# Performance work log

Hardware: AMD Instinct MI355X
Metric: run time of the kernel (lower is better)

Reference implementation:

```python
import jax, jax.numpy as jnp
import numpy as np

LORA_RANK = 16
LORA_ALPHA = 16
LORA_SCALE = LORA_ALPHA / LORA_RANK


def setup_inputs() -> dict:
    key = jax.random.key(0)
    k1, k2, k3, k4, k5 = jax.random.split(key, 5)
    B, S, D_IN, D_OUT, N_LORA, R = 8, 2048, 4096, 4096, 3, LORA_RANK
    std = 1.0 / np.sqrt(D_IN)
    x = jax.random.normal(k1, (B, S, D_IN), dtype=jnp.float32)
    weight = jax.random.truncated_normal(k2, -3.0, 3.0, (D_OUT, D_IN), dtype=jnp.float32) * std
    bias = jax.random.normal(k3, (D_OUT,), dtype=jnp.float32) * 0.01
    lora_A = jax.random.normal(k4, (N_LORA, R, D_IN), dtype=jnp.float32) * std
    lora_B = jax.random.normal(k5, (N_LORA, D_OUT, R), dtype=jnp.float32) * 0.02
    # segment starts: samples 0-1 -> no LoRA (index 0 reserved), 2-3 -> adapter 1, 4-5 -> adapter 2, 6-7 -> adapter 3
    lora_start_indices = jnp.arange(4, dtype=jnp.int64) * 2
    return {"x": x, "weight": weight, "bias": bias, "lora_A": lora_A,
            "lora_B": lora_B, "lora_start_indices": lora_start_indices}


def reference(x, weight, bias, lora_A, lora_B, lora_start_indices):
    # Base linear: y = x @ W^T + b   (torch: weight @ x_column)
    y = jnp.einsum('bsd,od->bso', x, weight) + bias  # [B,S,D_out]
    B = x.shape[0]
    # Map each batch sample to its segment (SGMV-style dispatch over contiguous segments).
    seg = jnp.searchsorted(lora_start_indices, jnp.arange(B), side='right') - 1  # [B], 0 = no LoRA
    adapter_idx = jnp.clip(seg - 1, 0, lora_A.shape[0] - 1)
    A = lora_A[adapter_idx]   # [B, r, D_in]  (tiny gather)
    Bw = lora_B[adapter_idx]  # [B, D_out, r]
    lo = jnp.einsum('bsr,bor->bso', jnp.einsum('bsd,brd->bsr', x, A), Bw) * LORA_SCALE
    use_lora = (seg > 0)[:, None, None]
    return y + jnp.where(use_lora, lo, jnp.zeros((), dtype=y.dtype))
```

## Files before the change

kernel.cpp:

```cpp
#include <hip/hip_runtime.h>


typedef __attribute__((ext_vector_type(8))) short short8;
typedef __attribute__((ext_vector_type(4))) float f32x4;
typedef __attribute__((ext_vector_type(4))) unsigned short u16x4;
typedef unsigned short u16;

typedef __attribute__((address_space(1))) void as1_void;
typedef __attribute__((address_space(3))) void as3_void;

#define M_DIM 16384
#define N_DIM 4096
#define K_DIM 4096
#define K2 8192
#define BM 256
#define BN 256
#define BK 64

__device__ __forceinline__ u16 f2bf(float f) {
  union { float f; unsigned u; } v; v.f = f;
  unsigned r = (v.u + 0x7FFFu + ((v.u >> 16) & 1u)) >> 16;
  return (u16)r;
}
__device__ __forceinline__ float bf2f(u16 u) {
  union { unsigned u; float f; } v; v.u = ((unsigned)u) << 16;
  return v.f;
}
__device__ __forceinline__ void gload16(const void* g, void* lds) {
  __builtin_amdgcn_global_load_lds((as1_void*)g, (as3_void*)lds, 16, 0, 0);
}
__device__ __forceinline__ int seg_of_batch(const int* starts, int b) {
  int seg = -1;
#pragma unroll
  for (int i = 0; i < 4; ++i) seg += (starts[i] <= b) ? 1 : 0;
  return seg;
}

#define VMCNT(n) asm volatile("s_waitcnt vmcnt(" #n ")" ::: "memory")

__global__ __launch_bounds__(256) void prep_kernel(
    const float* __restrict__ x, const float* __restrict__ wgt,
    const float* __restrict__ lA, const float* __restrict__ lB,
    u16* __restrict__ xbf, u16* __restrict__ wbf,
    u16* __restrict__ abf, u16* __restrict__ bw) {
  const long long NX4 = 16777216LL;
  const long long NW4 = 4194304LL;
  const long long NA4 = 49152LL;
  const long long NB  = 12288LL;
  const long long total = NX4 + NW4 + NA4 + NB;
  const f32x4* x4 = (const f32x4*)x;
  const f32x4* w4 = (const f32x4*)wgt;
  const f32x4* a4 = (const f32x4*)lA;
  u16x4* xo = (u16x4*)xbf;
  u16x4* wo = (u16x4*)wbf;
  u16x4* ao = (u16x4*)abf;
  for (long long i = (long long)blockIdx.x * blockDim.x + threadIdx.x; i < total;
       i += (long long)gridDim.x * blockDim.x) {
    if (i < NX4) {
      f32x4 v = x4[i];
      u16x4 o = {f2bf(v.x), f2bf(v.y), f2bf(v.z), f2bf(v.w)};
      xo[i] = o;
    } else if (i < NX4 + NW4) {
      long long j = i - NX4;
      f32x4 v = w4[j];
      u16x4 o = {f2bf(v.x), f2bf(v.y), f2bf(v.z), f2bf(v.w)};
      wo[j] = o;
    } else if (i < NX4 + NW4 + NA4) {
      long long j = i - NX4 - NW4;
      f32x4 v = a4[j];
      u16x4 o = {f2bf(v.x), f2bf(v.y), f2bf(v.z), f2bf(v.w)};
      ao[j] = o;
    } else {
      long long p = i - NX4 - NW4 - NA4;
      const float* src = lB + p * 16;
      u16* dst = bw + p * 32;
#pragma unroll
      for (int j = 0; j < 16; ++j) dst[j] = f2bf(src[j]);
#pragma unroll
      for (int j = 16; j < 32; ++j) dst[j] = 0;
    }
  }
}

__global__ __launch_bounds__(256) void ucompute_kernel(
    const u16* __restrict__ xbf, const u16* __restrict__ abf,
    const int* __restrict__ starts, u16* __restrict__ u) {
  const int l = threadIdx.x & 63;
  const int w = threadIdx.x >> 6;
  const int mbase = blockIdx.x * 16 + w * 4;
  const int b = mbase >> 11;
  const int seg = seg_of_batch(starts, b);
  const int use = seg > 0;
  int ad = seg - 1; ad = ad < 0 ? 0 : (ad > 2 ? 2 : ad);

  float acc[4][16];
#pragma unroll
  for (int row = 0; row < 4; ++row)
#pragma unroll
    for (int r = 0; r < 16; ++r) acc[row][r] = 0.f;

  if (use) {
    const u16* xr = xbf + (size_t)mbase * K_DIM + l * 8;
    const u16* ar = abf + (size_t)ad * (16 * K_DIM) + l * 8;
    for (int pass = 0; pass < 8; ++pass) {
      const int off = pass * 512;
      float xv[4][8];
#pragma unroll
      for (int row = 0; row < 4; ++row) {
        short8 xs = *(const short8*)(xr + (size_t)row * K_DIM + off);
#pragma unroll
        for (int j = 0; j < 8; ++j) xv[row][j] = bf2f((u16)xs[j]);
      }
#pragma unroll
      for (int r = 0; r < 16; ++r) {
        short8 av = *(const short8*)(ar + (size_t)r * K_DIM + off);
#pragma unroll
        for (int j = 0; j < 8; ++j) {
          float a = bf2f((u16)av[j]);
#pragma unroll
          for (int row = 0; row < 4; ++row) acc[row][r] += xv[row][j] * a;
        }
      }
    }
  }
#pragma unroll
  for (int row = 0; row < 4; ++row) {
    float myval = 0.f;
#pragma unroll
    for (int r = 0; r < 16; ++r) {
      float v = acc[row][r];
      v += __shfl_xor(v, 32);
      v += __shfl_xor(v, 16);
      v += __shfl_xor(v, 8);
      v += __shfl_xor(v, 4);
      v += __shfl_xor(v, 2);
      v += __shfl_xor(v, 1);
      if (l == r) myval = v;
    }
    if (l < 32) u[(size_t)(mbase + row) * 32 + l] = (l < 16) ? f2bf(myval) : (u16)0;
  }
}


#define STAGE_A(buf, ih, kt) do { \
  gload16(aSrc + (size_t)((ih)*64) * K2 + (size_t)(kt)*128, \
          &As[buf][((ih)*64) * BK] + w * 512); \
  gload16(aSrc + (size_t)((ih)*64 + 128) * K2 + (size_t)(kt)*128, \
          &As[buf][((ih)*64 + 128) * BK] + w * 512); \
} while (0)
#define STAGE_B(buf, jh, kt) do { \
  gload16(bSrc + (size_t)((jh)*32) * K2 + (size_t)(kt)*128, \
          &Bs[buf][((jh)*32 + (w >> 2)*64) * BK] + (w & 3) * 512); \
  gload16(bSrc + (size_t)((jh)*32 + 128) * K2 + (size_t)(kt)*128, \
          &Bs[buf][((jh)*32 + (w >> 2)*64 + 128) * BK] + (w & 3) * 512); \
} while (0)

#define PHASE(buf, ih, jh, LA, LB, BARR, STAGE_STMT, WAIT_STMT) do { \
  if (LA) { \
    _Pragma("unroll") \
    for (int i2 = 0; i2 < 4; ++i2) { \
      const u16* ar = &As[buf][(wr*128 + (ih)*64 + i2*16 + fm) * BK]; \
      aFr[i2][0] = *(const short8*)(ar + c0); \
      aFr[i2][1] = *(const short8*)(ar + c1); \
    } \
  } \
  if (LB) { \
    _Pragma("unroll") \
    for (int j2 = 0; j2 < 2; ++j2) { \
      const u16* br = &Bs[buf][(wc*64 + (jh)*32 + j2*16 + fm) * BK]; \
      BARR[j2][0] = *(const short8*)(br + c0); \
      BARR[j2][1] = *(const short8*)(br + c1); \
    } \
  } \
  STAGE_STMT; \
  WAIT_STMT; \
  __builtin_amdgcn_s_barrier(); \
  __builtin_amdgcn_s_setprio(1); \
  _Pragma("unroll") \
  for (int i2 = 0; i2 < 4; ++i2) \
  _Pragma("unroll") \
  for (int j2 = 0; j2 < 2; ++j2) { \
    acc[(ih)*4 + i2][(jh)*2 + j2] = __builtin_amdgcn_mfma_f32_16x16x32_bf16( \
        aFr[i2][0], BARR[j2][0], acc[(ih)*4 + i2][(jh)*2 + j2], 0, 0, 0); \
    acc[(ih)*4 + i2][(jh)*2 + j2] = __builtin_amdgcn_mfma_f32_16x16x32_bf16( \
        aFr[i2][1], BARR[j2][1], acc[(ih)*4 + i2][(jh)*2 + j2], 0, 0, 0); \
  } \
  __builtin_amdgcn_s_setprio(0); \
  __builtin_amdgcn_s_barrier(); \
} while (0)

__global__ __launch_bounds__(512, 2) void gemm8_kernel(
    const u16* __restrict__ xbf, const u16* __restrict__ wbf,
    const float* __restrict__ bias, const u16* __restrict__ ubuf,
    const u16* __restrict__ bwpad, const int* __restrict__ starts,
    float* __restrict__ out) {
  __shared__ u16 As[2][BM * BK];
  __shared__ u16 Bs[2][BN * BK];

  const int tid = threadIdx.x;
  const int l = tid & 63;
  const int w = tid >> 6;

  const int bid = blockIdx.x;
  const int nb = (bid & 7) * 128 + (bid >> 3);
  const int m0 = (nb >> 4) << 8;
  const int n0 = (nb & 15) << 8;

  const int b = m0 >> 11;
  const int seg = seg_of_batch(starts, b);
  int ad = seg - 1; ad = ad < 0 ? 0 : (ad > 2 ? 2 : ad);

  const int lrow = l >> 3;
  const int swzslot = (l & 7) ^ lrow;
  const char* aSrc = (const char*)xbf +
      (size_t)(m0 + 8 * w + lrow) * K2 + swzslot * 16;
  const char* bSrc = (const char*)wbf +
      (size_t)(n0 + (w >> 2) * 64 + (w & 3) * 8 + lrow) * K2 + swzslot * 16;

  const int fm = l & 15;
  const int q = l >> 4;
  const int wr = w >> 2;
  const int wc = w & 3;
  const int c0 = ((q ^ (fm & 7)) * 8);
  const int c1 = (((q + 4) ^ (fm & 7)) * 8);

  f32x4 acc[8][4];
  const f32x4 z4 = {0.f, 0.f, 0.f, 0.f};
#pragma unroll
  for (int i = 0; i < 8; ++i)
#pragma unroll
    for (int j = 0; j < 4; ++j) acc[i][j] = z4;

  short8 aFr[4][2];
  short8 bF0r[2][2];
  short8 bF1r[2][2];

  STAGE_A(0, 0, 0); STAGE_B(0, 0, 0); STAGE_B(0, 1, 0); STAGE_A(0, 1, 0);
  STAGE_A(1, 0, 1); STAGE_B(1, 1, 1); STAGE_A(1, 1, 1);
  VMCNT(6);
  __builtin_amdgcn_s_barrier();

  for (int s = 0; s < 32; ++s) {
    const int t1 = 2 * s + 1;
    const int t2 = 2 * s + 2;
    const int t3 = 2 * s + 3;
    const bool more = (s < 31);
    PHASE(0, 0, 0, 1, 1, bF0r, STAGE_B(1, 0, t1), (void)0);
    PHASE(0, 0, 1, 0, 1, bF1r, if (more) STAGE_A(0, 0, t2), (void)0);
    PHASE(0, 1, 1, 1, 0, bF1r, if (more) STAGE_B(0, 1, t2), (void)0);
    PHASE(0, 1, 0, 0, 0, bF0r, if (more) STAGE_A(0, 1, t2),
          if (more) VMCNT(6); else VMCNT(0));
    PHASE(1, 0, 0, 1, 1, bF0r, if (more) STAGE_B(0, 0, t2), (void)0);
    PHASE(1, 0, 1, 0, 1, bF1r, if (more) STAGE_A(1, 0, t3), (void)0);
    PHASE(1, 1, 1, 1, 0, bF1r, if (more) STAGE_B(1, 1, t3), (void)0);
    PHASE(1, 1, 0, 0, 0, bF0r, if (more) STAGE_A(1, 1, t3),
          if (more) VMCNT(6); else VMCNT(0));
  }

  {
    u16* la = &As[0][0];
    u16* lb = &Bs[0][0];
    const int ls = l & 3;
    const int lr = l >> 2;
    const char* uSrc = (const char*)ubuf +
        (size_t)(m0 + 16 * w + lr) * 64 + ls * 16;
    const char* vSrc = (const char*)bwpad +
        ((size_t)ad * N_DIM + n0 + 16 * w + lr) * 64 + ls * 16;
    gload16(uSrc, la + (16 * w) * 32);
    gload16(uSrc + (size_t)128 * 64, la + (128 + 16 * w) * 32);
    gload16(vSrc, lb + (16 * w) * 32);
    gload16(vSrc + (size_t)128 * 64, lb + (128 + 16 * w) * 32);
    VMCNT(0);
    __builtin_amdgcn_s_barrier();
    short8 aF[8], bF[4];
#pragma unroll
    for (int i = 0; i < 8; ++i)
      aF[i] = *(const short8*)(la + (wr * 128 + i * 16 + fm) * 32 + q * 8);
#pragma unroll
    for (int j = 0; j < 4; ++j)
      bF[j] = *(const short8*)(lb + (wc * 64 + j * 16 + fm) * 32 + q * 8);
#pragma unroll
    for (int i = 0; i < 8; ++i)
#pragma unroll
      for (int j = 0; j < 4; ++j)
        acc[i][j] = __builtin_amdgcn_mfma_f32_16x16x32_bf16(aF[i], bF[j],
                                                            acc[i][j], 0, 0, 0);
  }

  float bv[4];
#pragma unroll
  for (int j = 0; j < 4; ++j) bv[j] = bias[n0 + wc * 64 + j * 16 + fm];
#pragma unroll
  for (int i = 0; i < 8; ++i) {
#pragma unroll
    for (int ii = 0; ii < 4; ++ii) {
      const int m = m0 + wr * 128 + i * 16 + q * 4 + ii;
      float* orow = out + (size_t)m * N_DIM + n0 + wc * 64 + fm;
#pragma unroll
      for (int j = 0; j < 4; ++j) orow[j * 16] = acc[i][j][ii] + bv[j];
    }
  }
}

__global__ __launch_bounds__(256) void u_f32_kernel(
    const float* __restrict__ x, const float* __restrict__ lA,
    const int* __restrict__ starts, float* __restrict__ u) {
  const int l = threadIdx.x & 63;
  const int w = threadIdx.x >> 6;
  const int m = blockIdx.x * 4 + w;
  const int b = m >> 11;
  const int seg = seg_of_batch(starts, b);
  const int use = seg > 0;
  int ad = seg - 1; ad = ad < 0 ? 0 : (ad > 2 ? 2 : ad);
  float acc[16];
#pragma unroll
  for (int r = 0; r < 16; ++r) acc[r] = 0.f;
  if (use) {
    const float* xr = x + (size_t)m * K_DIM + l * 4;
    const float* ar = lA + (size_t)ad * (16 * K_DIM) + l * 4;
    for (int pass = 0; pass < 16; ++pass) {
      const int off = pass * 256;
      f32x4 xv = *(const f32x4*)(xr + off);
#pragma unroll
      for (int r = 0; r < 16; ++r) {
        f32x4 av = *(const f32x4*)(ar + (size_t)r * K_DIM + off);
        acc[r] += xv.x * av.x + xv.y * av.y + xv.z * av.z + xv.w * av.w;
      }
    }
  }
  float myval = 0.f;
#pragma unroll
  for (int r = 0; r < 16; ++r) {
    float v = acc[r];
    v += __shfl_xor(v, 32);
    v += __shfl_xor(v, 16);
    v += __shfl_xor(v, 8);
    v += __shfl_xor(v, 4);
    v += __shfl_xor(v, 2);
    v += __shfl_xor(v, 1);
    if (l == r) myval = v;
  }
  if (l < 16) u[(size_t)m * 16 + l] = myval;
}

__global__ __launch_bounds__(256) void gemm_f32_fallback(
    const float* __restrict__ x, const float* __restrict__ wgt,
    const float* __restrict__ bias, const float* __restrict__ lB,
    const float* __restrict__ u, const int* __restrict__ starts,
    float* __restrict__ out) {
  __shared__ float xs[4096];
  const int m = blockIdx.y;
  const int n0 = blockIdx.x * 256;
  const int t = threadIdx.x;
  const f32x4* xr4 = (const f32x4*)(x + (size_t)m * K_DIM);
  f32x4* xs4 = (f32x4*)xs;
  for (int i = t; i < 1024; i += 256) xs4[i] = xr4[i];
  __syncthreads();
  const int b = m >> 11;
  const int seg = seg_of_batch(starts, b);
  const int use = seg > 0;
  int ad = seg - 1; ad = ad < 0 ? 0 : (ad > 2 ? 2 : ad);
  const int n = n0 + t;
  const f32x4* wr = (const f32x4*)(wgt + (size_t)n * K_DIM);
  float acc = 0.f;
  for (int kk = 0; kk < 1024; ++kk) {
    f32x4 wv = wr[kk];
    f32x4 xv = xs4[kk];
    acc += xv.x * wv.x + xv.y * wv.y + xv.z * wv.z + xv.w * wv.w;
  }
  acc += bias[n];
  if (use) {
    const float* Bn = lB + ((size_t)ad * N_DIM + n) * 16;
    const float* um = u + (size_t)m * 16;
    float lo = 0.f;
#pragma unroll
    for (int r = 0; r < 16; ++r) lo += um[r] * Bn[r];
    acc += lo;
  }
  out[(size_t)m * N_DIM + n] = acc;
}

extern "C" void kernel_launch(void* const* d_in, const int* in_sizes, int n_in,
                              void* d_out, int out_size, void* d_ws, size_t ws_size,
                              hipStream_t stream) {
  const float* x    = (const float*)d_in[0];
  const float* wgt  = (const float*)d_in[1];
  const float* bias = (const float*)d_in[2];
  const float* lA   = (const float*)d_in[3];
  const float* lB   = (const float*)d_in[4];
  const int* starts = (const int*)d_in[5];
  float* out = (float*)d_out;

  const size_t XBF_OFF = 0;
  const size_t WBF_OFF = 134217728;
  const size_t ABF_OFF = 167772160;
  const size_t BW_OFF  = 168165376;
  const size_t U_OFF   = 168951808;
  const size_t WS_NEEDED = 170000384;

  if (ws_size >= WS_NEEDED) {
    u16* xbf = (u16*)((char*)d_ws + XBF_OFF);
    u16* wbf = (u16*)((char*)d_ws + WBF_OFF);
    u16* abf = (u16*)((char*)d_ws + ABF_OFF);
    u16* bw  = (u16*)((char*)d_ws + BW_OFF);
    u16* u   = (u16*)((char*)d_ws + U_OFF);
    prep_kernel<<<8192, 256, 0, stream>>>(x, wgt, lA, lB, xbf, wbf, abf, bw);
    ucompute_kernel<<<1024, 256, 0, stream>>>(xbf, abf, starts, u);
    gemm8_kernel<<<1024, 512, 0, stream>>>(xbf, wbf, bias, u, bw, starts, out);
  } else {
    float* uf = (float*)d_ws;
    u_f32_kernel<<<4096, 256, 0, stream>>>(x, lA, starts, uf);
    gemm_f32_fallback<<<dim3(16, 16384), 256, 0, stream>>>(x, wgt, bias, lB, uf, starts, out);
  }
}
```

Baseline: 1.132 ms.

## Software-pipeline LDS fragment reads one phase ahead of MFMA

Restructures the 8-phase GEMM main loop so LDS reads of A/B fragments for the next phase are issued before the current phase's MFMAs, using double-buffered register fragments (aF0r/aF1r, bF0A/bF0B). The aim is to hide LDS read latency behind matrix-core work instead of serializing reads, barrier and MFMA. This costs extra VGPRs for the additional fragment buffers, which at launch bounds (512,2) may cause spills. It also relies on the barrier placement correctly protecting buffers that are overwritten while reads are in flight.

```diff
diff --git a/kernel.cpp b/kernel.cpp
--- a/kernel.cpp
+++ b/kernel.cpp
@@ -37,6 +37,7 @@
 }
 
 #define VMCNT(n) asm volatile("s_waitcnt vmcnt(" #n ")" ::: "memory")
+#define BAR() __builtin_amdgcn_s_barrier()
 
 __global__ __launch_bounds__(256) void prep_kernel(
     const float* __restrict__ x, const float* __restrict__ wgt,
@@ -155,38 +156,35 @@
           &Bs[buf][((jh)*32 + (w >> 2)*64 + 128) * BK] + (w & 3) * 512); \
 } while (0)
 
-#define PHASE(buf, ih, jh, LA, LB, BARR, STAGE_STMT, WAIT_STMT) do { \
-  if (LA) { \
-    _Pragma("unroll") \
-    for (int i2 = 0; i2 < 4; ++i2) { \
-      const u16* ar = &As[buf][(wr*128 + (ih)*64 + i2*16 + fm) * BK]; \
-      aFr[i2][0] = *(const short8*)(ar + c0); \
-      aFr[i2][1] = *(const short8*)(ar + c1); \
-    } \
+#define READ_A(dst, buf, ih) do { \
+  _Pragma("unroll") \
+  for (int i2 = 0; i2 < 4; ++i2) { \
+    const u16* ar = &As[buf][(wr*128 + (ih)*64 + i2*16 + fm) * BK]; \
+    dst[i2][0] = *(const short8*)(ar + c0); \
+    dst[i2][1] = *(const short8*)(ar + c1); \
   } \
-  if (LB) { \
-    _Pragma("unroll") \
-    for (int j2 = 0; j2 < 2; ++j2) { \
-      const u16* br = &Bs[buf][(wc*64 + (jh)*32 + j2*16 + fm) * BK]; \
-      BARR[j2][0] = *(const short8*)(br + c0); \
-      BARR[j2][1] = *(const short8*)(br + c1); \
-    } \
+} while (0)
+#define READ_B(dst, buf, jh) do { \
+  _Pragma("unroll") \
+  for (int j2 = 0; j2 < 2; ++j2) { \
+    const u16* br = &Bs[buf][(wc*64 + (jh)*32 + j2*16 + fm) * BK]; \
+    dst[j2][0] = *(const short8*)(br + c0); \
+    dst[j2][1] = *(const short8*)(br + c1); \
   } \
-  STAGE_STMT; \
-  WAIT_STMT; \
-  __builtin_amdgcn_s_barrier(); \
+} while (0)
+
+#define MFMA16(ih, jh, A, B) do { \
   __builtin_amdgcn_s_setprio(1); \
   _Pragma("unroll") \
   for (int i2 = 0; i2 < 4; ++i2) \
   _Pragma("unroll") \
   for (int j2 = 0; j2 < 2; ++j2) { \
     acc[(ih)*4 + i2][(jh)*2 + j2] = __builtin_amdgcn_mfma_f32_16x16x32_bf16( \
-        aFr[i2][0], BARR[j2][0], acc[(ih)*4 + i2][(jh)*2 + j2], 0, 0, 0); \
+        A[i2][0], B[j2][0], acc[(ih)*4 + i2][(jh)*2 + j2], 0, 0, 0); \
     acc[(ih)*4 + i2][(jh)*2 + j2] = __builtin_amdgcn_mfma_f32_16x16x32_bf16( \
-        aFr[i2][1], BARR[j2][1], acc[(ih)*4 + i2][(jh)*2 + j2], 0, 0, 0); \
+        A[i2][1], B[j2][1], acc[(ih)*4 + i2][(jh)*2 + j2], 0, 0, 0); \
   } \
   __builtin_amdgcn_s_setprio(0); \
-  __builtin_amdgcn_s_barrier(); \
 } while (0)
 
 __global__ __launch_bounds__(512, 2) void gemm8_kernel(
@@ -231,30 +229,76 @@
 #pragma unroll
     for (int j = 0; j < 4; ++j) acc[i][j] = z4;
 
-  short8 aFr[4][2];
-  short8 bF0r[2][2];
+  short8 aF0r[4][2];
+  short8 aF1r[4][2];
+  short8 bF0A[2][2];
+  short8 bF0B[2][2];
   short8 bF1r[2][2];
 
   STAGE_A(0, 0, 0); STAGE_B(0, 0, 0); STAGE_B(0, 1, 0); STAGE_A(0, 1, 0);
   STAGE_A(1, 0, 1); STAGE_B(1, 1, 1); STAGE_A(1, 1, 1);
   VMCNT(6);
-  __builtin_amdgcn_s_barrier();
+  BAR();
+  READ_A(aF0r, 0, 0);
+  READ_B(bF0B, 0, 0);
 
   for (int s = 0; s < 32; ++s) {
     const int t1 = 2 * s + 1;
     const int t2 = 2 * s + 2;
     const int t3 = 2 * s + 3;
     const bool more = (s < 31);
-    PHASE(0, 0, 0, 1, 1, bF0r, STAGE_B(1, 0, t1), (void)0);
-    PHASE(0, 0, 1, 0, 1, bF1r, if (more) STAGE_A(0, 0, t2), (void)0);
-    PHASE(0, 1, 1, 1, 0, bF1r, if (more) STAGE_B(0, 1, t2), (void)0);
-    PHASE(0, 1, 0, 0, 0, bF0r, if (more) STAGE_A(0, 1, t2),
-          if (more) VMCNT(6); else VMCNT(0));
-    PHASE(1, 0, 0, 1, 1, bF0r, if (more) STAGE_B(0, 0, t2), (void)0);
-    PHASE(1, 0, 1, 0, 1, bF1r, if (more) STAGE_A(1, 0, t3), (void)0);
-    PHASE(1, 1, 1, 1, 0, bF1r, if (more) STAGE_B(1, 1, t3), (void)0);
-    PHASE(1, 1, 0, 0, 0, bF0r, if (more) STAGE_A(1, 1, t3),
-          if (more) VMCNT(6); else VMCNT(0));
+
+    STAGE_B(1, 0, t1);
+    BAR();
+    READ_B(bF1r, 0, 1);
+    MFMA16(0, 0, aF0r, bF0B);
+    BAR();
+
+    if (more) STAGE_A(0, 0, t2);
+    BAR();
+    READ_A(aF1r, 0, 1);
+    MFMA16(0, 1, aF0r, bF1r);
+    BAR();
+
+    if (more) STAGE_B(0, 1, t2);
+    BAR();
+    MFMA16(1, 1, aF1r, bF1r);
+    BAR();
+
+    if (more) STAGE_A(0, 1, t2);
+    if (more) { VMCNT(6); } else { VMCNT(0); }
+    BAR();
+    READ_A(aF0r, 1, 0);
+    READ_B(bF0A, 1, 0);
+    MFMA16(1, 0, aF1r, bF0B);
+    BAR();
+
+    if (more) STAGE_B(0, 0, t2);
+    BAR();
+    READ_B(bF1r, 1, 1);
+    MFMA16(0, 0, aF0r, bF0A);
+    BAR();
+
+    if (more) STAGE_A(1, 0, t3);
+    BAR();
+    READ_A(aF1r, 1, 1);
+    MFMA16(0, 1, aF0r, bF1r);
+    BAR();
+
+    if (more) STAGE_B(1, 1, t3);
+    BAR();
+    MFMA16(1, 1, aF1r, bF1r);
+    BAR();
+
+    if (more) STAGE_A(1, 1, t3);
+    if (more) { VMCNT(6); } else { VMCNT(0); }
+    BAR();
+    if (more) {
+      READ_A(aF0r, 0, 0);
+      READ_B(bF0B, 0, 0);
+    }
+    MFMA16(1, 0, aF1r, bF0A);
+    BAR();
   }
 
   {
@@ -271,7 +315,7 @@
     gload16(vSrc, lb + (16 * w) * 32);
     gload16(vSrc + (size_t)128 * 64, lb + (128 + 16 * w) * 32);
     VMCNT(0);
-    __builtin_amdgcn_s_barrier();
+    BAR();
     short8 aF[8], bF[4];
 #pragma unroll
     for (int i = 0; i < 8; ++i)
```

Measured after the change: 1.211 ms. 1.07x slower.
